# Performance work log

Hardware: AMD Instinct MI355X
Metric: run time of the kernel (lower is better)

## Reference

```python
import jax, jax.numpy as jnp
import numpy as np


def setup_inputs() -> dict:
    key = jax.random.key(0)
    ks = jax.random.split(key, 9)
    V, D, C, B = 100000, 128, 10, 16384
    return {
        "target_w_id": jax.random.randint(ks[0], (B,), 0, V),
        "context_w_ids": jax.random.randint(ks[1], (B, C), 0, V),
        "R": jax.random.normal(ks[2], (V, D), dtype=jnp.float32),
        "M_w": jax.random.normal(ks[3], (2 * D, 2 * D), dtype=jnp.float32) * 0.05,
        "M_b": jax.random.normal(ks[4], (2 * D,), dtype=jnp.float32) * 0.05,
        "U_w": jax.random.normal(ks[5], (D, 2 * D), dtype=jnp.float32) * 0.05,
        "U_b": jax.random.normal(ks[6], (D,), dtype=jnp.float32) * 0.05,
        "W_w": jax.random.normal(ks[7], (D, 2 * D), dtype=jnp.float32) * 0.05,
        "W_b": jax.random.normal(ks[8], (D,), dtype=jnp.float32) * 0.05,
    }


def reference(target_w_id, context_w_ids, R, M_w, M_b, U_w, U_b, W_w, W_b):
    # Gather embeddings: tw [B, D], cw [B, C, D]
    tw = R[target_w_id]
    cw = R[context_w_ids]
    B, C, D = cw.shape
    # Concat context embed with (broadcast) target embed -> [B, C, 2D]
    tw_b = jnp.broadcast_to(tw[:, None, :], (B, C, D))
    stacked = jnp.concatenate([cw, tw_b], axis=-1)
    # Linear M (torch: x @ W.T + b), ReLU, sum over context window -> h [B, 2D]
    proj = jnp.einsum("bcd,ed->bce", stacked, M_w) + M_b
    h = jnp.sum(jax.nn.relu(proj), axis=1)
    posterior_mu = h @ U_w.T + U_b
    posterior_sigma = jax.nn.softplus(h @ W_w.T + W_b)
    return (posterior_mu, posterior_sigma)
```

## Files before the change

kernel.cpp:

```cpp
#include <hip/hip_runtime.h>
#include <hip/hip_bf16.h>

typedef __attribute__((ext_vector_type(8))) short short8;
typedef __attribute__((ext_vector_type(4))) float floatx4;

static __device__ __forceinline__ short f2bf(float f) {
    union { float f; unsigned u; } v; v.f = f;
    unsigned r = v.u + 0x7fffu + ((v.u >> 16) & 1u);
    return (short)(r >> 16);
}
static __device__ __forceinline__ float bf2f(short s) {
    union { unsigned u; float f; } v; v.u = ((unsigned)(unsigned short)s) << 16;
    return v.f;
}

#define C_CTX 10
#define D_EMB 128
#define E_DIM 256

__global__ void prep_main(const float* __restrict__ Mw, const float* __restrict__ Uw,
                          const float* __restrict__ Ww, short* __restrict__ M1f,
                          short* __restrict__ M2f, short* __restrict__ B2f)
{
    int u = blockIdx.x * 256 + threadIdx.x;
    const float* src;
    short* dst;
    if (u < 8192) {
        int f = u & 4095;
        int l = f & 63, kc = (f >> 6) & 3, grp = f >> 8;
        int e = grp * 16 + (l & 15);
        int k = kc * 32 + (l >> 4) * 8 + ((u < 4096) ? 0 : 128);
        src = Mw + (size_t)e * E_DIM + k;
        dst = ((u < 4096) ? M1f : M2f) + (size_t)f * 8;
    } else {
        int f = u - 8192;
        int l = f & 63, ni = (f >> 6) & 3, kc = (f >> 8) & 7, w = f >> 11;
        int e = w * 64 + ni * 16 + (l & 15);
        int k = kc * 32 + (l >> 4) * 8;
        src = (e < 128) ? (Uw + (size_t)e * E_DIM + k)
                        : (Ww + (size_t)(e - 128) * E_DIM + k);
        dst = B2f + (size_t)f * 8;
    }
    float4 x = *(const float4*)src;
    float4 y = *(const float4*)(src + 4);
    short8 o;
    o[0]=f2bf(x.x); o[1]=f2bf(x.y); o[2]=f2bf(x.z); o[3]=f2bf(x.w);
    o[4]=f2bf(y.x); o[5]=f2bf(y.y); o[6]=f2bf(y.z); o[7]=f2bf(y.w);
    *(short8*)dst = o;
}

__global__ __launch_bounds__(256, 4)
void k_gt2(const float* __restrict__ R, const short* __restrict__ M1f,
           const short* __restrict__ M2f, const float* __restrict__ Mb,
           const int* __restrict__ tgt, short* __restrict__ G,
           short* __restrict__ Ttb, int V, int NG)
{
    __shared__ __align__(16) short buf[64 * 264];
    __shared__ int tids[64];
    const int t = threadIdx.x, w = t >> 6, l = t & 63;
    const bool isG = (int)blockIdx.x < NG;
    const int r0 = (isG ? blockIdx.x : (blockIdx.x - NG)) * 64;

    if (!isG && t < 64) tids[t] = tgt[r0 + t];
    if (!isG) __syncthreads();

    #pragma unroll
    for (int i = 0; i < 4; ++i) {
        int fa = t + i * 256;
        int li = fa & 63, frag = fa >> 6;
        int kc = frag >> 2, mi = frag & 3;
        int r = mi * 16 + (li & 15);
        int k = kc * 32 + (li >> 4) * 8;
        int gr;
        if (isG) { gr = r0 + r; if (gr >= V) gr = V - 1; }
        else     { gr = tids[r]; }
        const float* s = R + (size_t)gr * D_EMB + k;
        float4 x = *(const float4*)s;
        float4 y = *(const float4*)(s + 4);
        short8 v;
        v[0]=f2bf(x.x); v[1]=f2bf(x.y); v[2]=f2bf(x.z); v[3]=f2bf(x.w);
        v[4]=f2bf(y.x); v[5]=f2bf(y.y); v[6]=f2bf(y.z); v[7]=f2bf(y.w);
        *(short8*)&buf[fa * 8] = v;
    }
    __syncthreads();

    const short* Bf = isG ? M1f : M2f;
    floatx4 acc[4][4];
    #pragma unroll
    for (int mi = 0; mi < 4; ++mi)
        #pragma unroll
        for (int ni = 0; ni < 4; ++ni)
            acc[mi][ni] = (floatx4){0.f, 0.f, 0.f, 0.f};

    #pragma unroll
    for (int kc = 0; kc < 4; ++kc) {
        short8 afr[4], bfr[4];
        #pragma unroll
        for (int mi = 0; mi < 4; ++mi)
            afr[mi] = *(const short8*)&buf[((kc * 4 + mi) * 64 + l) * 8];
        #pragma unroll
        for (int ni = 0; ni < 4; ++ni)
            bfr[ni] = *(const short8*)(Bf + (((size_t)(w * 4 + ni) * 4 + kc) * 64 + l) * 8);
        #pragma unroll
        for (int mi = 0; mi < 4; ++mi)
            #pragma unroll
            for (int ni = 0; ni < 4; ++ni)
                acc[mi][ni] = __builtin_amdgcn_mfma_f32_16x16x32_bf16(afr[mi], bfr[ni], acc[mi][ni], 0, 0, 0);
    }
    __syncthreads();

    #pragma unroll
    for (int mi = 0; mi < 4; ++mi)
        #pragma unroll
        for (int ni = 0; ni < 4; ++ni) {
            int col = w * 64 + ni * 16 + (l & 15);
            float bias = isG ? 0.f : Mb[col];
            #pragma unroll
            for (int j = 0; j < 4; ++j) {
                int row = mi * 16 + (l >> 4) * 4 + j;
                buf[row * 264 + col] = f2bf(acc[mi][ni][j] + bias);
            }
        }
    __syncthreads();

    short* dst = isG ? G : Ttb;
    #pragma unroll
    for (int i = 0; i < 8; ++i) {
        int u = t + i * 256;
        int row = u >> 5, c8 = (u & 31) * 8;
        int gr = r0 + row;
        if (!isG || gr < V)
            *(short8*)(dst + (size_t)gr * 256 + c8) = *(const short8*)&buf[row * 264 + c8];
    }
}

__global__ __launch_bounds__(256, 4)
void k_hh(const int* __restrict__ ctx, const short* __restrict__ G,
          const short* __restrict__ Ttb, const short* __restrict__ B2f,
          const float* __restrict__ Ub, const float* __restrict__ Wb,
          float* __restrict__ out, int Bsz)
{
    __shared__ __align__(16) short hfr[8 * 64 * 8];
    __shared__ int ids[16 * C_CTX];
    const int t = threadIdx.x, w = t >> 6, l = t & 63;
    const int b0 = blockIdx.x * 16;

    if (t < 16 * C_CTX) ids[t] = ctx[(size_t)b0 * C_CTX + t];
    __syncthreads();

    const int hw = l >> 5;
    const int i5 = l & 31;
    const int kcc = i5 & 7, sub = i5 >> 3;
    const int c8 = kcc * 32 + sub * 8;

    #pragma unroll
    for (int p = 0; p < 2; ++p) {
        int bl = p * 8 + w * 2 + hw;
        short8 tr = *(const short8*)(Ttb + (size_t)(b0 + bl) * E_DIM + c8);
        float tv[8], acc[8];
        #pragma unroll
        for (int j = 0; j < 8; ++j) { tv[j] = bf2f(tr[j]); acc[j] = 0.f; }
        #pragma unroll
        for (int c = 0; c < C_CTX; ++c) {
            short8 g = *(const short8*)(G + (size_t)ids[bl * C_CTX + c] * E_DIM + c8);
            #pragma unroll
            for (int j = 0; j < 8; ++j)
                acc[j] += fmaxf(bf2f(g[j]) + tv[j], 0.f);
        }
        int sp = (sub * 16 + bl) ^ kcc;
        short8 o;
        #pragma unroll
        for (int j = 0; j < 8; ++j) o[j] = f2bf(acc[j]);
        *(short8*)&hfr[(kcc * 64 + sp) * 8] = o;
    }
    __syncthreads();

    floatx4 acc2[4];
    #pragma unroll
    for (int ni = 0; ni < 4; ++ni)
        acc2[ni] = (floatx4){0.f, 0.f, 0.f, 0.f};

    #pragma unroll
    for (int kc = 0; kc < 8; ++kc) {
        short8 afr = *(const short8*)&hfr[(kc * 64 + (l ^ kc)) * 8];
        short8 bfr[4];
        #pragma unroll
        for (int ni = 0; ni < 4; ++ni)
            bfr[ni] = *(const short8*)(B2f + ((((size_t)w * 8 + kc) * 4 + ni) * 64 + l) * 8);
        #pragma unroll
        for (int ni = 0; ni < 4; ++ni)
            acc2[ni] = __builtin_amdgcn_mfma_f32_16x16x32_bf16(afr, bfr[ni], acc2[ni], 0, 0, 0);
    }

    #pragma unroll
    for (int ni = 0; ni < 4; ++ni) {
        int col = w * 64 + ni * 16 + (l & 15);
        #pragma unroll
        for (int j = 0; j < 4; ++j) {
            int rr = (l >> 4) * 4 + j;
            int r = b0 + rr;
            float v = acc2[ni][j];
            if (col < 128) {
                out[(size_t)r * 128 + col] = v + Ub[col];
            } else {
                float xx = v + Wb[col - 128];
                float sp = fmaxf(xx, 0.f) + log1pf(expf(-fabsf(xx)));
                out[(size_t)Bsz * 128 + (size_t)r * 128 + (col - 128)] = sp;
            }
        }
    }
}

extern "C" void kernel_launch(void* const* d_in, const int* in_sizes, int n_in,
                              void* d_out, int out_size, void* d_ws, size_t ws_size,
                              hipStream_t stream)
{
    const int*   tgt = (const int*)d_in[0];
    const int*   ctx = (const int*)d_in[1];
    const float* R   = (const float*)d_in[2];
    const float* Mw  = (const float*)d_in[3];
    const float* Mb  = (const float*)d_in[4];
    const float* Uw  = (const float*)d_in[5];
    const float* Ub  = (const float*)d_in[6];
    const float* Ww  = (const float*)d_in[7];
    const float* Wb  = (const float*)d_in[8];
    float* out = (float*)d_out;
    const int Bsz = in_sizes[0];
    const int Vn  = in_sizes[2] / D_EMB;

    char* ws = (char*)d_ws;
    size_t offG   = 0;
    size_t offT   = offG + (size_t)Vn * 512;
    size_t offM1f = offT + (size_t)Bsz * 512;
    size_t offM2f = offM1f + 65536;
    size_t offB2f = offM2f + 65536;

    short* G   = (short*)(ws + offG);
    short* Ttb = (short*)(ws + offT);
    short* M1f = (short*)(ws + offM1f);
    short* M2f = (short*)(ws + offM2f);
    short* B2f = (short*)(ws + offB2f);

    const int NG = (Vn + 63) / 64;
    const int NT = Bsz / 64;

    prep_main<<<64, 256, 0, stream>>>(Mw, Uw, Ww, M1f, M2f, B2f);
    k_gt2<<<NG + NT, 256, 0, stream>>>(R, M1f, M2f, Mb, tgt, G, Ttb, Vn, NG);
    k_hh<<<Bsz / 16, 256, 0, stream>>>(ctx, G, Ttb, B2f, Ub, Wb, out, Bsz);
}
```

Before: 64.28 us.

## Store projected vocab table in FP8 with permuted column layout, drop LDS staging

The precomputed per-vocab projection G is now stored as FP8 instead of bf16, which halves the bytes written over the whole 100k-row table and the bytes read by the context gather. Results are written straight from MFMA accumulators in a column-permuted order, so the LDS transpose and its barriers go away. The permutation is undone in the K dimension of the second-stage weights (B2f) and of the Ttb layout. This adds FP8 quantization error to the pre-ReLU values, which may hurt accuracy, and the stores become narrower per-thread writes.

```diff
diff --git a/kernel.cpp b/kernel.cpp
--- a/kernel.cpp
+++ b/kernel.cpp
@@ -3,6 +3,7 @@
 
 typedef __attribute__((ext_vector_type(8))) short short8;
 typedef __attribute__((ext_vector_type(4))) float floatx4;
+typedef __attribute__((ext_vector_type(2))) float floatx2;
 
 static __device__ __forceinline__ short f2bf(float f) {
     union { float f; unsigned u; } v; v.f = f;
@@ -18,44 +19,48 @@
 #define D_EMB 128
 #define E_DIM 256
 
+
 __global__ void prep_main(const float* __restrict__ Mw, const float* __restrict__ Uw,
                           const float* __restrict__ Ww, short* __restrict__ M1f,
                           short* __restrict__ M2f, short* __restrict__ B2f)
 {
     int u = blockIdx.x * 256 + threadIdx.x;
-    const float* src;
-    short* dst;
     if (u < 8192) {
         int f = u & 4095;
         int l = f & 63, kc = (f >> 6) & 3, grp = f >> 8;
         int e = grp * 16 + (l & 15);
         int k = kc * 32 + (l >> 4) * 8 + ((u < 4096) ? 0 : 128);
-        src = Mw + (size_t)e * E_DIM + k;
-        dst = ((u < 4096) ? M1f : M2f) + (size_t)f * 8;
+        const float* src = Mw + (size_t)e * E_DIM + k;
+        float4 x = *(const float4*)src;
+        float4 y = *(const float4*)(src + 4);
+        short8 o;
+        o[0]=f2bf(x.x); o[1]=f2bf(x.y); o[2]=f2bf(x.z); o[3]=f2bf(x.w);
+        o[4]=f2bf(y.x); o[5]=f2bf(y.y); o[6]=f2bf(y.z); o[7]=f2bf(y.w);
+        *(short8*)(((u < 4096) ? M1f : M2f) + (size_t)f * 8) = o;
     } else {
         int f = u - 8192;
         int l = f & 63, ni = (f >> 6) & 3, kc = (f >> 8) & 7, w = f >> 11;
         int e = w * 64 + ni * 16 + (l & 15);
-        int k = kc * 32 + (l >> 4) * 8;
-        src = (e < 128) ? (Uw + (size_t)e * E_DIM + k)
-                        : (Ww + (size_t)(e - 128) * E_DIM + k);
-        dst = B2f + (size_t)f * 8;
-    }
-    float4 x = *(const float4*)src;
-    float4 y = *(const float4*)(src + 4);
-    short8 o;
-    o[0]=f2bf(x.x); o[1]=f2bf(x.y); o[2]=f2bf(x.z); o[3]=f2bf(x.w);
-    o[4]=f2bf(y.x); o[5]=f2bf(y.y); o[6]=f2bf(y.z); o[7]=f2bf(y.w);
-    *(short8*)dst = o;
+        const float* src = (e < 128) ? (Uw + (size_t)e * E_DIM)
+                                     : (Ww + (size_t)(e - 128) * E_DIM);
+        short8 o;
+        #pragma unroll
+        for (int i = 0; i < 8; ++i) {
+            int pk = kc * 32 + (l >> 4) * 8 + i;
+            int ok = (pk >> 6) * 64 + (pk & 3) * 16 + ((pk >> 2) & 15);
+            o[i] = f2bf(src[ok]);
+        }
+        *(short8*)(B2f + (size_t)f * 8) = o;
+    }
 }
 
 __global__ __launch_bounds__(256, 4)
 void k_gt2(const float* __restrict__ R, const short* __restrict__ M1f,
            const short* __restrict__ M2f, const float* __restrict__ Mb,
-           const int* __restrict__ tgt, short* __restrict__ G,
+           const int* __restrict__ tgt, unsigned char* __restrict__ G8,
            short* __restrict__ Ttb, int V, int NG)
 {
-    __shared__ __align__(16) short buf[64 * 264];
+    __shared__ __align__(16) short buf[1024 * 8];
     __shared__ int tids[64];
     const int t = threadIdx.x, w = t >> 6, l = t & 63;
     const bool isG = (int)blockIdx.x < NG;
@@ -107,35 +112,41 @@
             for (int ni = 0; ni < 4; ++ni)
                 acc[mi][ni] = __builtin_amdgcn_mfma_f32_16x16x32_bf16(afr[mi], bfr[ni], acc[mi][ni], 0, 0, 0);
     }
-    __syncthreads();
-
-    #pragma unroll
-    for (int mi = 0; mi < 4; ++mi)
-        #pragma unroll
-        for (int ni = 0; ni < 4; ++ni) {
-            int col = w * 64 + ni * 16 + (l & 15);
-            float bias = isG ? 0.f : Mb[col];
+
+    const int pcb = w * 64 + (l & 15) * 4;
+    if (isG) {
+        #pragma unroll
+        for (int mi = 0; mi < 4; ++mi)
             #pragma unroll
             for (int j = 0; j < 4; ++j) {
-                int row = mi * 16 + (l >> 4) * 4 + j;
-                buf[row * 264 + col] = f2bf(acc[mi][ni][j] + bias);
+                int row = r0 + mi * 16 + (l >> 4) * 4 + j;
+                if (row < V) {
+                    int u = __builtin_amdgcn_cvt_pk_fp8_f32(acc[mi][0][j], acc[mi][1][j], 0, false);
+                    u = __builtin_amdgcn_cvt_pk_fp8_f32(acc[mi][2][j], acc[mi][3][j], u, true);
+                    *(int*)(G8 + (size_t)row * 256 + pcb) = u;
+                }
             }
-        }
-    __syncthreads();
-
-    short* dst = isG ? G : Ttb;
-    #pragma unroll
-    for (int i = 0; i < 8; ++i) {
-        int u = t + i * 256;
-        int row = u >> 5, c8 = (u & 31) * 8;
-        int gr = r0 + row;
-        if (!isG || gr < V)
-            *(short8*)(dst + (size_t)gr * 256 + c8) = *(const short8*)&buf[row * 264 + c8];
+    } else {
+        float mb[4];
+        #pragma unroll
+        for (int ni = 0; ni < 4; ++ni) mb[ni] = Mb[w * 64 + ni * 16 + (l & 15)];
+        #pragma unroll
+        for (int mi = 0; mi < 4; ++mi)
+            #pragma unroll
+            for (int j = 0; j < 4; ++j) {
+                int row = r0 + mi * 16 + (l >> 4) * 4 + j;
+                unsigned u0 = ((unsigned)(unsigned short)f2bf(acc[mi][1][j] + mb[1]) << 16)
+                            |  (unsigned)(unsigned short)f2bf(acc[mi][0][j] + mb[0]);
+                unsigned u1 = ((unsigned)(unsigned short)f2bf(acc[mi][3][j] + mb[3]) << 16)
+                            |  (unsigned)(unsigned short)f2bf(acc[mi][2][j] + mb[2]);
+                uint2 uv; uv.x = u0; uv.y = u1;
+                *(uint2*)(Ttb + (size_t)row * 256 + pcb) = uv;
+            }
     }
 }
 
 __global__ __launch_bounds__(256, 4)
-void k_hh(const int* __restrict__ ctx, const short* __restrict__ G,
+void k_hh(const int* __restrict__ ctx, const unsigned char* __restrict__ G8,
           const short* __restrict__ Ttb, const short* __restrict__ B2f,
           const float* __restrict__ Ub, const float* __restrict__ Wb,
           float* __restrict__ out, int Bsz)
@@ -162,10 +173,19 @@
         for (int j = 0; j < 8; ++j) { tv[j] = bf2f(tr[j]); acc[j] = 0.f; }
         #pragma unroll
         for (int c = 0; c < C_CTX; ++c) {
-            short8 g = *(const short8*)(G + (size_t)ids[bl * C_CTX + c] * E_DIM + c8);
-            #pragma unroll
-            for (int j = 0; j < 8; ++j)
-                acc[j] += fmaxf(bf2f(g[j]) + tv[j], 0.f);
+            uint2 g = *(const uint2*)(G8 + (size_t)ids[bl * C_CTX + c] * E_DIM + c8);
+            floatx2 d01 = __builtin_amdgcn_cvt_pk_f32_fp8((int)g.x, false);
+            floatx2 d23 = __builtin_amdgcn_cvt_pk_f32_fp8((int)g.x, true);
+            floatx2 d45 = __builtin_amdgcn_cvt_pk_f32_fp8((int)g.y, false);
+            floatx2 d67 = __builtin_amdgcn_cvt_pk_f32_fp8((int)g.y, true);
+            acc[0] += fmaxf(d01[0] + tv[0], 0.f);
+            acc[1] += fmaxf(d01[1] + tv[1], 0.f);
+            acc[2] += fmaxf(d23[0] + tv[2], 0.f);
+            acc[3] += fmaxf(d23[1] + tv[3], 0.f);
+            acc[4] += fmaxf(d45[0] + tv[4], 0.f);
+            acc[5] += fmaxf(d45[1] + tv[5], 0.f);
+            acc[6] += fmaxf(d67[0] + tv[6], 0.f);
+            acc[7] += fmaxf(d67[1] + tv[7], 0.f);
         }
         int sp = (sub * 16 + bl) ^ kcc;
         short8 o;
@@ -230,12 +250,12 @@
 
     char* ws = (char*)d_ws;
     size_t offG   = 0;
-    size_t offT   = offG + (size_t)Vn * 512;
+    size_t offT   = offG + (size_t)Vn * 256;
     size_t offM1f = offT + (size_t)Bsz * 512;
     size_t offM2f = offM1f + 65536;
     size_t offB2f = offM2f + 65536;
 
-    short* G   = (short*)(ws + offG);
+    unsigned char* G8 = (unsigned char*)(ws + offG);
     short* Ttb = (short*)(ws + offT);
     short* M1f = (short*)(ws + offM1f);
     short* M2f = (short*)(ws + offM2f);
@@ -245,6 +265,6 @@
     const int NT = Bsz / 64;
 
     prep_main<<<64, 256, 0, stream>>>(Mw, Uw, Ww, M1f, M2f, B2f);
-    k_gt2<<<NG + NT, 256, 0, stream>>>(R, M1f, M2f, Mb, tgt, G, Ttb, Vn, NG);
-    k_hh<<<Bsz / 16, 256, 0, stream>>>(ctx, G, Ttb, B2f, Ub, Wb, out, Bsz);
-}
+    k_gt2<<<NG + NT, 256, 0, stream>>>(R, M1f, M2f, Mb, tgt, G8, Ttb, Vn, NG);
+    k_hh<<<Bsz / 16, 256, 0, stream>>>(ctx, G8, Ttb, B2f, Ub, Wb, out, Bsz);
+}
```

Result: faster. 53.93 us (-16.1%).
